# Kernel tuning notes

Hardware: AMD Instinct MI355X
Metric: run time of the kernel (lower is better)

Reference implementation:

```python
import jax, jax.numpy as jnp
import numpy as np

N = 100000   # nodes
D = 16       # fixed neighbor-set size (regular graph)
H = 128      # h_feats
L = 2        # num_iterations (stacked SAGEConv layers)
C = 10       # num_outputs


def setup_inputs() -> dict:
    key = jax.random.key(0)
    ks = jax.random.split(key, 20)
    s = 1.0 / np.sqrt(H)
    u = lambda k, shp: jax.random.uniform(k, shp, jnp.float32, -s, s)
    inp = {
        "h": jax.random.normal(ks[0], (N, H), jnp.float32),
        "nbr": jax.random.randint(ks[1], (N, D), 0, N, jnp.int32),
        # per-layer SAGEConv(lstm) params, stacked over L
        "lstm_Wih": u(ks[2], (L, 4 * H, H)),
        "lstm_Whh": u(ks[3], (L, 4 * H, H)),
        "lstm_b":   u(ks[4], (L, 4 * H)),   # b_ih + b_hh folded together
        "Wself":    u(ks[5], (L, H, H)),
        "bself":    u(ks[6], (L, H)),
        "Wneigh":   u(ks[7], (L, H, H)),
        "bneigh":   u(ks[8], (L, H)),
        "cls_W":  u(ks[9], (5, H, H)),
        "cls_b":  u(ks[10], (5, H)),
        "cls_oW": u(ks[11], (C, H)),
        "cls_ob": u(ks[12], (C,)),
        # cnf head: same but final Linear H->1
        "cnf_W":  u(ks[13], (5, H, H)),
        "cnf_b":  u(ks[14], (5, H)),
        "cnf_oW": u(ks[15], (1, H)),
        "cnf_ob": u(ks[16], (1,)),
    }
    return inp


def _sage_lstm_layer(h, nbr, Wih, Whh, b, Ws, bs, Wn, bn):
    """DGL SAGEConv with 'lstm' aggregator over a fixed-degree neighbor list.
    LSTM (PyTorch gate order i,f,g,o) runs over the D neighbors of every node;
    the final hidden state is the neighborhood aggregate."""
    hs0 = jnp.zeros((h.shape[0], H), h.dtype)
    cs0 = jnp.zeros_like(hs0)

    def step(carry, idx_row):            # idx_row: [N] neighbor ids at step t
        hs, cs = carry
        x = h[idx_row]                   # gather neighbor features [N, H]
        gates = x @ Wih.T + hs @ Whh.T + b
        i, f, g, o = jnp.split(gates, 4, axis=-1)
        cs = jax.nn.sigmoid(f) * cs + jax.nn.sigmoid(i) * jnp.tanh(g)
        hs = jax.nn.sigmoid(o) * jnp.tanh(cs)
        return (hs, cs), None

    (h_neigh, _), _ = jax.lax.scan(step, (hs0, cs0), nbr.T)  # scan over D steps
    return jax.nn.relu(h @ Ws.T + bs + h_neigh @ Wn.T + bn)


def _mlp_head(x, W, bvec, oW, ob):
    for i in range(5):
        x = jax.nn.relu(x @ W[i].T + bvec[i])   # Dropout(0.2) is identity in eval
    return x @ oW.T + ob


def reference(h, nbr, lstm_Wih, lstm_Whh, lstm_b, Wself, bself, Wneigh, bneigh,
              cls_W, cls_b, cls_oW, cls_ob, cnf_W, cnf_b, cnf_oW, cnf_ob):
    for layer in range(L):
        h = _sage_lstm_layer(h, nbr, lstm_Wih[layer], lstm_Whh[layer], lstm_b[layer],
                             Wself[layer], bself[layer], Wneigh[layer], bneigh[layer])
    o = _mlp_head(h, cls_W, cls_b, cls_oW, cls_ob)   # [N, C]
    l = _mlp_head(h, cnf_W, cnf_b, cnf_oW, cnf_ob)   # [N, 1]
    return (o, h, l)
```

## Files before the change

kernel.cpp:

```cpp
#include <hip/hip_runtime.h>
#include <stdint.h>


typedef __attribute__((ext_vector_type(8))) short short8_t;
typedef __attribute__((ext_vector_type(4))) float float4_t;
typedef __attribute__((ext_vector_type(4))) unsigned uint4_t;
typedef _Float16 half8_t __attribute__((ext_vector_type(8)));

#define NNODES 100000
#define DNB 16
#define LOSCALE 32768.0f
#define LOINV   3.0517578125e-5f

__device__ __forceinline__ float fsigf(float x) {
    return __builtin_amdgcn_rcpf(1.f + __expf(-x));
}
__device__ __forceinline__ float ftanhf(float x) {
    return 1.f - 2.f * __builtin_amdgcn_rcpf(1.f + __expf(2.f * x));
}
__device__ __forceinline__ unsigned f2b(float f) {
    unsigned u = __float_as_uint(f);
    return (u + 0x7FFFu + ((u >> 16) & 1u)) >> 16;
}
__device__ __forceinline__ float blo(unsigned u) { return __uint_as_float(u << 16); }
__device__ __forceinline__ float bhi(unsigned u) { return __uint_as_float(u & 0xFFFF0000u); }
__device__ __forceinline__ unsigned pkhi(unsigned u0, unsigned u1) {
    return __builtin_amdgcn_perm(u1, u0, 0x07060302u);
}
__device__ __forceinline__ void splitf8(const float* __restrict__ p, short8_t& hi, short8_t& lo) {
    float4_t a = *(const float4_t*)p;
    float4_t b = *(const float4_t*)(p + 4);
#pragma unroll
    for (int j = 0; j < 8; ++j) {
        float x = j < 4 ? a[j] : b[j - 4];
        unsigned hb = f2b(x);
        float hf = __uint_as_float(hb << 16);
        unsigned lb = f2b(x - hf);
        hi[j] = (short)hb;
        lo[j] = (short)lb;
    }
}
__device__ __forceinline__ unsigned cvtpk(float lo, float hi) {
    unsigned r;
    asm("v_cvt_pk_bf16_f32 %0, %1, %2" : "=v"(r) : "v"(lo), "v"(hi));
    return r;
}
__device__ __forceinline__ void splitf8_pk(const float* __restrict__ p, short8_t& hi, short8_t& lo) {
    float4_t a = *(const float4_t*)p;
    float4_t b = *(const float4_t*)(p + 4);
    unsigned h0 = cvtpk(a[0], a[1]), h1 = cvtpk(a[2], a[3]);
    unsigned h2 = cvtpk(b[0], b[1]), h3 = cvtpk(b[2], b[3]);
    unsigned l0 = cvtpk(a[0] - blo(h0), a[1] - bhi(h0));
    unsigned l1 = cvtpk(a[2] - blo(h1), a[3] - bhi(h1));
    unsigned l2 = cvtpk(b[0] - blo(h2), b[1] - bhi(h2));
    unsigned l3 = cvtpk(b[2] - blo(h3), b[3] - bhi(h3));
    union { uint4_t u; short8_t s; } ch, cl;
    ch.u = (uint4_t){h0, h1, h2, h3};
    cl.u = (uint4_t){l0, l1, l2, l3};
    hi = ch.s;
    lo = cl.s;
}
__device__ __forceinline__ short8_t cvtb8(const float* __restrict__ p) {
    float4_t a = *(const float4_t*)p;
    float4_t b = *(const float4_t*)(p + 4);
    union { uint4_t u; short8_t s; } c;
    c.u = (uint4_t){cvtpk(a[0], a[1]), cvtpk(a[2], a[3]),
                    cvtpk(b[0], b[1]), cvtpk(b[2], b[3])};
    return c.s;
}

__global__ __launch_bounds__(256) void xgemm_split(
    const float* __restrict__ A, const float* __restrict__ B,
    const float* __restrict__ bias, _Float16* __restrict__ Chi,
    char* __restrict__ Clo)
{
    const int tid  = threadIdx.x;
    const int wave = tid >> 6, lane = tid & 63;
    const int l15  = lane & 15, quad = lane >> 4;
    const int r0   = blockIdx.y * 64 + wave * 16;
    const int c0   = blockIdx.x * 64;

    int arow = r0 + l15;
    if (arow >= NNODES) arow = NNODES - 1;

    float4_t acc[4];
#pragma unroll
    for (int ct = 0; ct < 4; ++ct) acc[ct] = (float4_t){0.f, 0.f, 0.f, 0.f};

#pragma unroll
    for (int kc = 0; kc < 4; ++kc) {
        const int kk = kc * 32 + quad * 8;
        short8_t ah, al;
        splitf8_pk(A + (size_t)arow * 128 + kk, ah, al);
#pragma unroll
        for (int ct = 0; ct < 4; ++ct) {
            short8_t bh, bl;
            splitf8_pk(B + (size_t)(c0 + ct * 16 + l15) * 128 + kk, bh, bl);
            acc[ct] = __builtin_amdgcn_mfma_f32_16x16x32_bf16(ah, bh, acc[ct], 0, 0, 0);
            acc[ct] = __builtin_amdgcn_mfma_f32_16x16x32_bf16(ah, bl, acc[ct], 0, 0, 0);
            acc[ct] = __builtin_amdgcn_mfma_f32_16x16x32_bf16(al, bh, acc[ct], 0, 0, 0);
        }
    }

#pragma unroll
    for (int ct = 0; ct < 4; ++ct) {
        int c = c0 + ct * 16 + l15;
        float bb = bias[c];
        const int jj = c & 127, gg = c >> 7;
#pragma unroll
        for (int r = 0; r < 4; ++r) {
            int rowo = r0 + quad * 4 + r;
            if (rowo < NNODES) {
                float v = acc[ct][r] + bb;
                _Float16 hi = (_Float16)v;
                float res = v - (float)hi;
                int q = (int)rintf(res * LOSCALE);
                q = q > 127 ? 127 : (q < -127 ? -127 : q);
                Chi[(size_t)rowo * 512 + jj * 4 + gg] = hi;
                Clo[(size_t)rowo * 512 + jj * 4 + gg] = (char)q;
            }
        }
    }
}

__global__ __launch_bounds__(512, 2) void lstm_comb(
    const _Float16* __restrict__ Xhi, const char* __restrict__ Xlo,
    const int* __restrict__ nbr, const float* __restrict__ Whh,
    const float* hin, const float* __restrict__ Ws,
    const float* __restrict__ Wn, const float* __restrict__ bs,
    const float* __restrict__ bn, float* hout)
{
    __shared__ short hsAhi[64 * 136], hsAlo[64 * 136];
    __shared__ short hsBhi[64 * 136], hsBlo[64 * 136];
    __shared__ int   nbrs[64 * 17];

    const int tid  = threadIdx.x;
    const int wave = tid >> 6, lane = tid & 63;
    const int l15  = lane & 15, quad = lane >> 4;
    const int n0   = blockIdx.x * 64;
    const int jb   = wave * 16;
    const int xoff = jb * 4 + quad * 16;

    for (int i = tid; i < 64 * 136 / 2; i += 512) {
        ((unsigned*)hsAhi)[i] = 0;
        ((unsigned*)hsAlo)[i] = 0;
    }
    for (int i = tid; i < 64 * DNB; i += 512) {
        int node = n0 + (i >> 4);
        if (node >= NNODES) node = NNODES - 1;
        nbrs[(i >> 4) * 17 + (i & 15)] = nbr[node * DNB + (i & 15)];
    }

    short8_t whi[4][4], wlo[4][4];
#pragma unroll
    for (int g = 0; g < 4; ++g)
#pragma unroll
        for (int kc = 0; kc < 4; ++kc)
            splitf8(Whh + (size_t)(g * 128 + jb + l15) * 128 + kc * 32 + quad * 8,
                    whi[g][kc], wlo[g][kc]);

    float cs[4][4], nh[4][4];
#pragma unroll
    for (int a = 0; a < 4; ++a)
#pragma unroll
        for (int b = 0; b < 4; ++b) { cs[a][b] = 0.f; nh[a][b] = 0.f; }

    __syncthreads();

#define XV(nt, r, g)                                                                \
    ((float)(((r) * 4 + (g)) < 8 ? xh0[nt][(r) * 4 + (g)] : xh1[nt][(r) * 4 + (g) - 8]) \
     + (float)((signed char)(xl4[nt][(r)] >> ((g) * 8))) * LOINV)

#define LSTM_STEP(rdHi, rdLo, wrHi, wrLo, T)                                        \
    {                                                                               \
        half8_t xh0[4], xh1[4]; uint4_t xl4[4];                                     \
        _Pragma("unroll")                                                           \
        for (int nt = 0; nt < 4; ++nt) {                                            \
            int gi = nbrs[(nt * 16 + l15) * 17 + (T)];                              \
            size_t xb = (size_t)gi * 512 + xoff;                                    \
            xh0[nt] = *(const half8_t*)(Xhi + xb);                                  \
            xh1[nt] = *(const half8_t*)(Xhi + xb + 8);                              \
            xl4[nt] = *(const uint4_t*)(Xlo + xb);                                  \
        }                                                                           \
        _Pragma("unroll")                                                           \
        for (int nt = 0; nt < 4; ++nt) {                                            \
            short8_t hfh[4], hfl[4];                                                \
            _Pragma("unroll")                                                       \
            for (int kc = 0; kc < 4; ++kc) {                                        \
                hfh[kc] = *(const short8_t*)&(rdHi)[(nt * 16 + l15) * 136 + kc * 32 + quad * 8]; \
                hfl[kc] = *(const short8_t*)&(rdLo)[(nt * 16 + l15) * 136 + kc * 32 + quad * 8]; \
            }                                                                       \
            float4_t ac[4];                                                         \
            _Pragma("unroll")                                                       \
            for (int g = 0; g < 4; ++g) {                                           \
                float4_t a = (float4_t){0.f, 0.f, 0.f, 0.f};                        \
                _Pragma("unroll")                                                   \
                for (int kc = 0; kc < 4; ++kc) {                                    \
                    a = __builtin_amdgcn_mfma_f32_16x16x32_bf16(whi[g][kc], hfh[kc], a, 0, 0, 0); \
                    a = __builtin_amdgcn_mfma_f32_16x16x32_bf16(whi[g][kc], hfl[kc], a, 0, 0, 0); \
                    a = __builtin_amdgcn_mfma_f32_16x16x32_bf16(wlo[g][kc], hfh[kc], a, 0, 0, 0); \
                }                                                                   \
                ac[g] = a;                                                          \
            }                                                                       \
            _Pragma("unroll")                                                       \
            for (int r = 0; r < 4; ++r) {                                           \
                float iv = ac[0][r] + XV(nt, r, 0);                                 \
                float fv = ac[1][r] + XV(nt, r, 1);                                 \
                float gv = ac[2][r] + XV(nt, r, 2);                                 \
                float ov = ac[3][r] + XV(nt, r, 3);                                 \
                float c = fsigf(fv) * cs[nt][r] + fsigf(iv) * ftanhf(gv);           \
                cs[nt][r] = c;                                                      \
                nh[nt][r] = fsigf(ov) * ftanhf(c);                                  \
            }                                                                       \
        }                                                                           \
        _Pragma("unroll")                                                           \
        for (int nt = 0; nt < 4; ++nt) {                                            \
                    \
                    \
            unsigned u0 = __float_as_uint(nh[nt][0]);                               \
            unsigned u1 = __float_as_uint(nh[nt][1]);                               \
            unsigned u2 = __float_as_uint(nh[nt][2]);                               \
            unsigned u3 = __float_as_uint(nh[nt][3]);                               \
            unsigned r0 = __float_as_uint(nh[nt][0] - bhi(u0));                     \
            unsigned r1 = __float_as_uint(nh[nt][1] - bhi(u1));                     \
            unsigned r2 = __float_as_uint(nh[nt][2] - bhi(u2));                     \
            unsigned r3 = __float_as_uint(nh[nt][3] - bhi(u3));                     \
            uint2 ph, pl;                                                           \
            ph.x = pkhi(u0, u1); ph.y = pkhi(u2, u3);                               \
            pl.x = pkhi(r0, r1); pl.y = pkhi(r2, r3);                               \
            const int o = (nt * 16 + l15) * 136 + jb + quad * 4;                    \
            *(uint2*)&(wrHi)[o] = ph;                                               \
            *(uint2*)&(wrLo)[o] = pl;                                               \
        }                                                                           \
        __syncthreads();                                                            \
    }

    for (int tp = 0; tp < 8; ++tp) {
        LSTM_STEP(hsAhi, hsAlo, hsBhi, hsBlo, 2 * tp);
        LSTM_STEP(hsBhi, hsBlo, hsAhi, hsAlo, 2 * tp + 1);
    }
#undef LSTM_STEP
#undef XV

    const int ng = wave & 3, ch = wave >> 2;
    const int nodeA = n0 + ng * 16 + l15;
    const int nclA  = nodeA < NNODES ? nodeA : NNODES - 1;
    short8_t ahh[4], ahl[4], anh[4], anl[4];
#pragma unroll
    for (int kc = 0; kc < 4; ++kc) {
        splitf8(hin + (size_t)nclA * 128 + kc * 32 + quad * 8, ahh[kc], ahl[kc]);
        anh[kc] = *(const short8_t*)&hsAhi[(ng * 16 + l15) * 136 + kc * 32 + quad * 8];
        anl[kc] = *(const short8_t*)&hsAlo[(ng * 16 + l15) * 136 + kc * 32 + quad * 8];
    }
    __syncthreads();

#pragma unroll
    for (int ct = 0; ct < 4; ++ct) {
        const int ctg = ch * 4 + ct;
        float4_t acc = (float4_t){0.f, 0.f, 0.f, 0.f};
#pragma unroll
        for (int kc = 0; kc < 4; ++kc) {
            const int kk = kc * 32 + quad * 8;
            short8_t bh, bl;
            splitf8(Ws + (size_t)(ctg * 16 + l15) * 128 + kk, bh, bl);
            acc = __builtin_amdgcn_mfma_f32_16x16x32_bf16(ahh[kc], bh, acc, 0, 0, 0);
            acc = __builtin_amdgcn_mfma_f32_16x16x32_bf16(ahh[kc], bl, acc, 0, 0, 0);
            acc = __builtin_amdgcn_mfma_f32_16x16x32_bf16(ahl[kc], bh, acc, 0, 0, 0);
            splitf8(Wn + (size_t)(ctg * 16 + l15) * 128 + kk, bh, bl);
            acc = __builtin_amdgcn_mfma_f32_16x16x32_bf16(anh[kc], bh, acc, 0, 0, 0);
            acc = __builtin_amdgcn_mfma_f32_16x16x32_bf16(anh[kc], bl, acc, 0, 0, 0);
            acc = __builtin_amdgcn_mfma_f32_16x16x32_bf16(anl[kc], bh, acc, 0, 0, 0);
        }
        const int c = ctg * 16 + l15;
        const float bb = bs[c] + bn[c];
#pragma unroll
        for (int r = 0; r < 4; ++r) {
            int rowo = n0 + ng * 16 + quad * 4 + r;
            if (rowo < NNODES) {
                float v = acc[r] + bb;
                hout[(size_t)rowo * 128 + c] = v > 0.f ? v : 0.f;
            }
        }
    }
}

__global__ __launch_bounds__(256) void heads_fused(
    const float* __restrict__ hsrc,
    const float* __restrict__ clsW, const float* __restrict__ clsb,
    const float* __restrict__ clsoW, const float* __restrict__ clsob,
    const float* __restrict__ cnfW, const float* __restrict__ cnfb,
    const float* __restrict__ cnfoW, const float* __restrict__ cnfob,
    float* __restrict__ oC, float* __restrict__ oL)
{
    __shared__ short xb[64 * 132];
    __shared__ short wb[128 * 132];

    const int tid  = threadIdx.x;
    const int wave = tid >> 6, lane = tid & 63;
    const int l15  = lane & 15, quad = lane >> 4;
    const int n0   = blockIdx.x * 64;

    {
        int row = tid >> 2, cb = (tid & 3) * 32;
        int rsrc = n0 + row; if (rsrc >= NNODES) rsrc = NNODES - 1;
        const float* src = hsrc + (size_t)rsrc * 128 + cb;
#pragma unroll
        for (int i = 0; i < 4; ++i)
            *(short8_t*)&xb[row * 132 + cb + i * 8] = cvtb8(src + i * 8);
    }

    for (int head = 0; head < 2; ++head) {
        const float* W  = head ? cnfW : clsW;
        const float* bv = head ? cnfb : clsb;

        if (head == 1) {
            __syncthreads();
            int row = tid >> 2, cb = (tid & 3) * 32;
            int rsrc = n0 + row; if (rsrc >= NNODES) rsrc = NNODES - 1;
            const float* src = hsrc + (size_t)rsrc * 128 + cb;
#pragma unroll
            for (int i = 0; i < 4; ++i)
                *(short8_t*)&xb[row * 132 + cb + i * 8] = cvtb8(src + i * 8);
        }

        for (int l = 0; l < 5; ++l) {
            __syncthreads();
            short8_t af[4];
#pragma unroll
            for (int kc = 0; kc < 4; ++kc)
                af[kc] = *(const short8_t*)&xb[(wave * 16 + l15) * 132 + kc * 32 + quad * 8];
            const float* Wl = W + (size_t)l * 16384;
#pragma unroll
            for (int i = 0; i < 8; ++i) {
                int e = i * 2048 + tid * 8;
                int r = e >> 7, c = e & 127;
                *(short8_t*)&wb[r * 132 + c] = cvtb8(Wl + e);
            }
            __syncthreads();
#pragma unroll
            for (int ct = 0; ct < 8; ++ct) {
                float4_t acc = (float4_t){0.f, 0.f, 0.f, 0.f};
#pragma unroll
                for (int kc = 0; kc < 4; ++kc) {
                    short8_t bf = *(const short8_t*)&wb[(ct * 16 + l15) * 132 + kc * 32 + quad * 8];
                    acc = __builtin_amdgcn_mfma_f32_16x16x32_bf16(af[kc], bf, acc, 0, 0, 0);
                }
                int c = ct * 16 + l15;
                float bb = bv[l * 128 + c];
#pragma unroll
                for (int r = 0; r < 4; ++r) {
                    float v = acc[r] + bb;
                    v = v > 0.f ? v : 0.f;
                    xb[(wave * 16 + quad * 4 + r) * 132 + c] = (short)f2b(v);
                }
            }
        }

        __syncthreads();
        short8_t af[4];
#pragma unroll
        for (int kc = 0; kc < 4; ++kc)
            af[kc] = *(const short8_t*)&xb[(wave * 16 + l15) * 132 + kc * 32 + quad * 8];
        if (head == 0) {
            int wr = l15 < 10 ? l15 : 9;
            float4_t acc = (float4_t){0.f, 0.f, 0.f, 0.f};
#pragma unroll
            for (int kc = 0; kc < 4; ++kc) {
                short8_t bh, bl;
                splitf8(clsoW + (size_t)wr * 128 + kc * 32 + quad * 8, bh, bl);
                acc = __builtin_amdgcn_mfma_f32_16x16x32_bf16(af[kc], bh, acc, 0, 0, 0);
                acc = __builtin_amdgcn_mfma_f32_16x16x32_bf16(af[kc], bl, acc, 0, 0, 0);
            }
            if (l15 < 10) {
                float bb = clsob[l15];
#pragma unroll
                for (int r = 0; r < 4; ++r) {
                    int row = n0 + wave * 16 + quad * 4 + r;
                    if (row < NNODES) oC[(size_t)row * 10 + l15] = acc[r] + bb;
                }
            }
        } else {
            float4_t acc = (float4_t){0.f, 0.f, 0.f, 0.f};
#pragma unroll
            for (int kc = 0; kc < 4; ++kc) {
                short8_t bh, bl;
                splitf8(cnfoW + kc * 32 + quad * 8, bh, bl);
                acc = __builtin_amdgcn_mfma_f32_16x16x32_bf16(af[kc], bh, acc, 0, 0, 0);
                acc = __builtin_amdgcn_mfma_f32_16x16x32_bf16(af[kc], bl, acc, 0, 0, 0);
            }
            if (l15 == 0) {
                float bb = cnfob[0];
#pragma unroll
                for (int r = 0; r < 4; ++r) {
                    int row = n0 + wave * 16 + quad * 4 + r;
                    if (row < NNODES) oL[row] = acc[r] + bb;
                }
            }
        }
    }
}

extern "C" void kernel_launch(void* const* d_in, const int* in_sizes, int n_in,
                              void* d_out, int out_size, void* d_ws, size_t ws_size,
                              hipStream_t stream)
{
    const float* h0     = (const float*)d_in[0];
    const int*   nbr    = (const int*)d_in[1];
    const float* Wih    = (const float*)d_in[2];
    const float* Whh    = (const float*)d_in[3];
    const float* lb     = (const float*)d_in[4];
    const float* Wself  = (const float*)d_in[5];
    const float* bself  = (const float*)d_in[6];
    const float* Wneigh = (const float*)d_in[7];
    const float* bneigh = (const float*)d_in[8];
    const float* clsW   = (const float*)d_in[9];
    const float* clsb   = (const float*)d_in[10];
    const float* clsoW  = (const float*)d_in[11];
    const float* clsob  = (const float*)d_in[12];
    const float* cnfW   = (const float*)d_in[13];
    const float* cnfb   = (const float*)d_in[14];
    const float* cnfoW  = (const float*)d_in[15];
    const float* cnfob  = (const float*)d_in[16];

    char* ws = (char*)d_ws;
    _Float16* Xhi = (_Float16*)ws;
    char*     Xlo = ws + 102400000;

    float* out = (float*)d_out;
    float* oC  = out;
    float* hO  = out + 1000000;
    float* oL  = out + 13800000;

    dim3 gx(8, 1563);
    dim3 gl(1563);
    dim3 gf(1563);

    xgemm_split<<<gx, dim3(256), 0, stream>>>(h0, Wih, lb, Xhi, Xlo);
    lstm_comb<<<gl, dim3(512), 0, stream>>>(Xhi, Xlo, nbr, Whh, h0,
                                            Wself, Wneigh, bself, bneigh, hO);
    xgemm_split<<<gx, dim3(256), 0, stream>>>(hO, Wih + 65536, lb + 512, Xhi, Xlo);
    lstm_comb<<<gl, dim3(512), 0, stream>>>(Xhi, Xlo, nbr, Whh + 65536, hO,
                                            Wself + 16384, Wneigh + 16384,
                                            bself + 128, bneigh + 128, hO);

    heads_fused<<<gf, dim3(256), 0, stream>>>(hO, clsW, clsb, clsoW, clsob,
                                              cnfW, cnfb, cnfoW, cnfob, oC, oL);
}
```

Before: 2.911 ms.

## Prefetch next-step neighbor gathers and prescale gates by log2e for exp2

Each LSTM step now issues the gather of the next timestep's precomputed input projections right after the gate math and before the LDS writeback and barrier. This lets the global-memory latency overlap with the sync instead of stalling at the start of every step. Gate pre-activations (both the precomputed X projection and the Whh weights) are prescaled by log2(e), or 2·log2(e) for the g gate, so the sigmoid and tanh use a raw exp2 without an extra multiply. The trade-off is higher register pressure from holding the prefetched tiles across the step, plus a slight change in rounding because the fp16+int8 split now stores scaled values.

```diff
diff --git a/kernel.cpp b/kernel.cpp
--- a/kernel.cpp
+++ b/kernel.cpp
@@ -11,12 +11,20 @@
 #define DNB 16
 #define LOSCALE 32768.0f
 #define LOINV   3.0517578125e-5f
-
-__device__ __forceinline__ float fsigf(float x) {
-    return __builtin_amdgcn_rcpf(1.f + __expf(-x));
-}
-__device__ __forceinline__ float ftanhf(float x) {
-    return 1.f - 2.f * __builtin_amdgcn_rcpf(1.f + __expf(2.f * x));
+#define L2E     1.4426950408889634f
+#define TWOL2E  2.8853900817779268f
+
+#if __has_builtin(__builtin_amdgcn_exp2f)
+#define EXP2(x) __builtin_amdgcn_exp2f(x)
+#else
+#define EXP2(x) __expf((x) * 0.6931471805599453f)
+#endif
+
+__device__ __forceinline__ float fsig2(float y) {
+    return __builtin_amdgcn_rcpf(1.f + EXP2(-y));
+}
+__device__ __forceinline__ float ftanh2(float y) {
+    return 1.f - 2.f * __builtin_amdgcn_rcpf(1.f + EXP2(y));
 }
 __device__ __forceinline__ unsigned f2b(float f) {
     unsigned u = __float_as_uint(f);
@@ -33,6 +41,20 @@
 #pragma unroll
     for (int j = 0; j < 8; ++j) {
         float x = j < 4 ? a[j] : b[j - 4];
+        unsigned hb = f2b(x);
+        float hf = __uint_as_float(hb << 16);
+        unsigned lb = f2b(x - hf);
+        hi[j] = (short)hb;
+        lo[j] = (short)lb;
+    }
+}
+__device__ __forceinline__ void splitf8s(const float* __restrict__ p, float s,
+                                         short8_t& hi, short8_t& lo) {
+    float4_t a = *(const float4_t*)p;
+    float4_t b = *(const float4_t*)(p + 4);
+#pragma unroll
+    for (int j = 0; j < 8; ++j) {
+        float x = (j < 4 ? a[j] : b[j - 4]) * s;
         unsigned hb = f2b(x);
         float hf = __uint_as_float(hb << 16);
         unsigned lb = f2b(x - hf);
@@ -107,11 +129,12 @@
         int c = c0 + ct * 16 + l15;
         float bb = bias[c];
         const int jj = c & 127, gg = c >> 7;
+        const float sc = (((c0 + ct * 16) >> 7) == 2) ? TWOL2E : L2E;
 #pragma unroll
         for (int r = 0; r < 4; ++r) {
             int rowo = r0 + quad * 4 + r;
             if (rowo < NNODES) {
-                float v = acc[ct][r] + bb;
+                float v = (acc[ct][r] + bb) * sc;
                 _Float16 hi = (_Float16)v;
                 float res = v - (float)hi;
                 int q = (int)rintf(res * LOSCALE);
@@ -150,14 +173,17 @@
         if (node >= NNODES) node = NNODES - 1;
         nbrs[(i >> 4) * 17 + (i & 15)] = nbr[node * DNB + (i & 15)];
     }
+    if (tid < 64) nbrs[tid * 17 + 16] = 0;
 
     short8_t whi[4][4], wlo[4][4];
 #pragma unroll
-    for (int g = 0; g < 4; ++g)
+    for (int g = 0; g < 4; ++g) {
+        const float sg = (g == 2) ? TWOL2E : L2E;
 #pragma unroll
         for (int kc = 0; kc < 4; ++kc)
-            splitf8(Whh + (size_t)(g * 128 + jb + l15) * 128 + kc * 32 + quad * 8,
-                    whi[g][kc], wlo[g][kc]);
+            splitf8s(Whh + (size_t)(g * 128 + jb + l15) * 128 + kc * 32 + quad * 8,
+                     sg, whi[g][kc], wlo[g][kc]);
+    }
 
     float cs[4][4], nh[4][4];
 #pragma unroll
@@ -166,14 +192,16 @@
         for (int b = 0; b < 4; ++b) { cs[a][b] = 0.f; nh[a][b] = 0.f; }
 
     __syncthreads();
+
+    half8_t xh0[4], xh1[4];
+    uint4_t xl4[4];
 
 #define XV(nt, r, g)                                                                \
     ((float)(((r) * 4 + (g)) < 8 ? xh0[nt][(r) * 4 + (g)] : xh1[nt][(r) * 4 + (g) - 8]) \
      + (float)((signed char)(xl4[nt][(r)] >> ((g) * 8))) * LOINV)
 
-#define LSTM_STEP(rdHi, rdLo, wrHi, wrLo, T)                                        \
+#define XLOADALL(T)                                                                 \
     {                                                                               \
-        half8_t xh0[4], xh1[4]; uint4_t xl4[4];                                     \
         _Pragma("unroll")                                                           \
         for (int nt = 0; nt < 4; ++nt) {                                            \
             int gi = nbrs[(nt * 16 + l15) * 17 + (T)];                              \
@@ -182,6 +210,10 @@
             xh1[nt] = *(const half8_t*)(Xhi + xb + 8);                              \
             xl4[nt] = *(const uint4_t*)(Xlo + xb);                                  \
         }                                                                           \
+    }
+
+#define LSTM_STEP(rdHi, rdLo, wrHi, wrLo, T)                                        \
+    {                                                                               \
         _Pragma("unroll")                                                           \
         for (int nt = 0; nt < 4; ++nt) {                                            \
             short8_t hfh[4], hfl[4];                                                \
@@ -208,15 +240,14 @@
                 float fv = ac[1][r] + XV(nt, r, 1);                                 \
                 float gv = ac[2][r] + XV(nt, r, 2);                                 \
                 float ov = ac[3][r] + XV(nt, r, 3);                                 \
-                float c = fsigf(fv) * cs[nt][r] + fsigf(iv) * ftanhf(gv);           \
+                float c = fsig2(fv) * cs[nt][r] + fsig2(iv) * ftanh2(gv);           \
                 cs[nt][r] = c;                                                      \
-                nh[nt][r] = fsigf(ov) * ftanhf(c);                                  \
+                nh[nt][r] = fsig2(ov) * ftanh2(c * TWOL2E);                         \
             }                                                                       \
         }                                                                           \
+        XLOADALL((T) + 1)                                                           \
         _Pragma("unroll")                                                           \
         for (int nt = 0; nt < 4; ++nt) {                                            \
-                    \
-                    \
             unsigned u0 = __float_as_uint(nh[nt][0]);                               \
             unsigned u1 = __float_as_uint(nh[nt][1]);                               \
             unsigned u2 = __float_as_uint(nh[nt][2]);                               \
@@ -235,11 +266,14 @@
         __syncthreads();                                                            \
     }
 
+    XLOADALL(0)
+
     for (int tp = 0; tp < 8; ++tp) {
         LSTM_STEP(hsAhi, hsAlo, hsBhi, hsBlo, 2 * tp);
         LSTM_STEP(hsBhi, hsBlo, hsAhi, hsAlo, 2 * tp + 1);
     }
 #undef LSTM_STEP
+#undef XLOADALL
 #undef XV
 
     const int ng = wave & 3, ch = wave >> 2;
```

New measurement: 4.093 ms. 1.41x slower.
